# Kernel optimization log

Measured on AMD Instinct MI355X. Metric: run time of the kernel, lower is better.

## Reference

```python
import jax, jax.numpy as jnp
import numpy as np

N = 50000
NEG_SLOPE = 0.2  # PyG GATConv default leaky_relu slope


def _gat_layer(x, src, dst, W, a_s, a_d, b):
    # x: [N, Fin]; W: [Fin, H*C]; a_s, a_d: [H, C]; b: [C]
    H, C = a_s.shape
    xp = (x @ W).reshape(N, H, C)                      # projected node features per head
    alpha_s = jnp.einsum('nhc,hc->nh', xp, a_s)        # [N, H]
    alpha_d = jnp.einsum('nhc,hc->nh', xp, a_d)        # [N, H]
    e = jax.nn.leaky_relu(alpha_s[src] + alpha_d[dst], NEG_SLOPE)  # [E, H]
    # segment softmax over incoming edges of each dst node
    m = jax.ops.segment_max(e, dst, num_segments=N)
    m = jnp.where(jnp.isfinite(m), m, 0.0)
    p = jnp.exp(e - jax.lax.stop_gradient(m)[dst])
    denom = jax.ops.segment_sum(p, dst, num_segments=N)
    alpha = p / denom[dst]                             # [E, H]
    # scatter-aggregate messages
    out = jax.ops.segment_sum(alpha[:, :, None] * xp[src], dst, num_segments=N)  # [N, H, C]
    return out.mean(axis=1) + b                        # concat=False -> mean over heads


def setup_inputs() -> dict:
    key = jax.random.key(0)
    ks = jax.random.split(key, 16)
    IN, HID, OUT, H = 128, 64, 40, 4
    E = 800000
    x = jax.random.normal(ks[0], (N, IN), dtype=jnp.float32)
    edge_index = jax.random.randint(ks[1], (2, E), 0, N, dtype=jnp.int64)

    def mk(kw, ka, fin, fout):
        s = 1.0 / np.sqrt(fin)
        W = jax.random.normal(kw, (fin, H * fout), dtype=jnp.float32) * s
        a_s = jax.random.normal(ka, (H, fout), dtype=jnp.float32) * 0.1
        a_d = jax.random.normal(jax.random.fold_in(ka, 1), (H, fout), dtype=jnp.float32) * 0.1
        b = jnp.zeros((fout,), dtype=jnp.float32)
        return W, a_s, a_d, b

    W1, as1, ad1, b1 = mk(ks[2], ks[3], IN, HID)
    W2, as2, ad2, b2 = mk(ks[4], ks[5], HID, HID)
    W3, as3, ad3, b3 = mk(ks[6], ks[7], HID, OUT)
    return dict(x=x, edge_index=edge_index,
                W1=W1, as1=as1, ad1=ad1, b1=b1,
                W2=W2, as2=as2, ad2=ad2, b2=b2,
                W3=W3, as3=as3, ad3=ad3, b3=b3)


def reference(x, edge_index, W1, as1, ad1, b1, W2, as2, ad2, b2, W3, as3, ad3, b3):
    # PyG GATConv adds self-loops by default
    loop = jnp.arange(N, dtype=edge_index.dtype)
    src = jnp.concatenate([edge_index[0], loop])
    dst = jnp.concatenate([edge_index[1], loop])
    h = jax.nn.relu(_gat_layer(x, src, dst, W1, as1, ad1, b1))   # dropout is identity in eval
    h = jax.nn.relu(_gat_layer(h, src, dst, W2, as2, ad2, b2))
    h = jax.nn.relu(_gat_layer(h, src, dst, W3, as3, ad3, b3))
    return jax.nn.log_softmax(h, axis=-1)
```

## Files before the change

### kernel.cpp

```cpp
#include <hip/hip_runtime.h>
#include <math.h>

#define NNODES 50000
#define NEG_SLOPE 0.2f
#define NBUCKET 391
#define CHUNK_MAX 12544
#define NBIN_MAX 128

typedef unsigned short ushort8v __attribute__((ext_vector_type(8)));
typedef unsigned short ushort4v __attribute__((ext_vector_type(4)));
typedef short short8v __attribute__((ext_vector_type(8)));
typedef float f32x4 __attribute__((ext_vector_type(4)));
typedef float f32x2 __attribute__((ext_vector_type(2)));

__device__ __forceinline__ unsigned short f2bf(float f){
    unsigned u = __float_as_uint(f);
    u += 0x7fff + ((u >> 16) & 1);
    return (unsigned short)(u >> 16);
}

__device__ __forceinline__ void emit_wa(const float* __restrict__ W, const float* __restrict__ a_s,
                                        const float* __restrict__ a_d, unsigned short* __restrict__ Wt,
                                        int Kin, int C, int id){
    const int n = id / Kin, k = id - n * Kin;
    float v = 0.f;
    if(n < 8){
        const int hh = n & 3;
        const float* av = (n < 4) ? a_s : a_d;
        for(int c = 0; c < C; c++) v += W[(size_t)k * (4 * C) + hh * C + c] * av[hh * C + c];
    }
    Wt[id] = f2bf(v);
}

__device__ __forceinline__ void emit_wc(const float* __restrict__ W, unsigned short* __restrict__ Wt,
                                        int Kin, int C, int id){
    const int c = id / (4 * Kin);
    const int hk = id - c * (4 * Kin);
    const int h = hk / Kin, k = hk - h * Kin;
    const float v = (c < C) ? W[(size_t)k * (4 * C) + h * C + c] * 0.25f : 0.f;
    Wt[id] = f2bf(v);
}

__global__ void initprep_kernel(const unsigned long long* __restrict__ e, int* __restrict__ flag,
                                const float* __restrict__ x, unsigned short* __restrict__ xbf, int X4,
                                const float* __restrict__ W1, const float* __restrict__ as1, const float* __restrict__ ad1,
                                const float* __restrict__ W2, const float* __restrict__ as2, const float* __restrict__ ad2,
                                const float* __restrict__ W3, const float* __restrict__ as3, const float* __restrict__ ad3,
                                unsigned short* __restrict__ Wa1, unsigned short* __restrict__ Wa2,
                                unsigned short* __restrict__ Wa3, unsigned short* __restrict__ Wc1,
                                unsigned short* __restrict__ Wc2, unsigned short* __restrict__ Wc3){
    if(blockIdx.x == 0 && threadIdx.x < 64){
        const unsigned long long v = e[threadIdx.x];
        const unsigned long long mask = __ballot(v >= (1ULL << 32));
        if(threadIdx.x == 0) *flag = (mask == 0ULL) ? 1 : 0;
    }
    int id = blockIdx.x * blockDim.x + threadIdx.x;
    if(id < X4){
        const float4 v = *(const float4*)&x[(size_t)id * 4];
        ushort4v o;
        o[0] = f2bf(v.x); o[1] = f2bf(v.y); o[2] = f2bf(v.z); o[3] = f2bf(v.w);
        *(ushort4v*)&xbf[(size_t)id * 4] = o;
        return;
    }
    id -= X4;
    if(id < 16 * 128){ emit_wa(W1, as1, ad1, Wa1, 128, 64, id); return; }
    id -= 16 * 128;
    if(id < 16 * 64){ emit_wa(W2, as2, ad2, Wa2, 64, 64, id); return; }
    id -= 16 * 64;
    if(id < 16 * 64){ emit_wa(W3, as3, ad3, Wa3, 64, 40, id); return; }
    id -= 16 * 64;
    if(id < 64 * 512){ emit_wc(W1, Wc1, 128, 64, id); return; }
    id -= 64 * 512;
    if(id < 64 * 256){ emit_wc(W2, Wc2, 64, 64, id); return; }
    id -= 64 * 256;
    if(id < 48 * 256){ emit_wc(W3, Wc3, 64, 40, id); }
}

__global__ __launch_bounds__(256) void bincount_kernel(const void* __restrict__ e, const int* __restrict__ flag,
                                                       int* __restrict__ blkcnt, int E, int nbin, int chunk){
    __shared__ int lcnt[NBUCKET];
    for(int i = threadIdx.x; i < NBUCKET; i += 256) lcnt[i] = 0;
    __syncthreads();
    const bool f = (*flag) != 0;
    const int beg = blockIdx.x * chunk;
    const int end = min(beg + chunk, E);
    for(int i = beg + threadIdx.x; i < end; i += 256){
        const int d = f ? (int)((const long long*)e)[E + i] : ((const int*)e)[E + i];
        atomicAdd(&lcnt[d >> 7], 1);
    }
    __syncthreads();
    for(int b = threadIdx.x; b < NBUCKET; b += 256)
        blkcnt[b * nbin + blockIdx.x] = lcnt[b];
}

__global__ __launch_bounds__(256) void binscan_kernel(int* __restrict__ blkcnt, int total){
    __shared__ int part[256];
    const int t = threadIdx.x;
    const int per = (total + 255) / 256;
    const int beg = t * per, end = min(beg + per, total);
    int sum = 0;
    for(int i = beg; i < end; i++) sum += blkcnt[i];
    part[t] = sum;
    __syncthreads();
    for(int off = 1; off < 256; off <<= 1){
        const int add = (t >= off) ? part[t - off] : 0;
        __syncthreads();
        part[t] += add;
        __syncthreads();
    }
    int run = part[t] - sum;
    for(int i = beg; i < end; i++){
        const int v = blkcnt[i];
        blkcnt[i] = run;
        run += v;
    }
}

__global__ __launch_bounds__(256) void binscatter_kernel(const void* __restrict__ e, const int* __restrict__ flag,
                                                         const int* __restrict__ blkcnt,
                                                         unsigned* __restrict__ ebuf,
                                                         int E, int nbin, int chunk){
    __shared__ unsigned stage[CHUNK_MAX];
    __shared__ unsigned sorted[CHUNK_MAX];
    __shared__ int lcnt[512], lsc[512];
    __shared__ int lcur[NBUCKET], gb[NBUCKET];
    const int t = threadIdx.x;
    const int blk = blockIdx.x;
    lcnt[t] = 0; lcnt[t + 256] = 0;
    __syncthreads();
    const bool f = (*flag) != 0;
    const int beg = blk * chunk;
    const int cnt = min(chunk, E - beg);
    for(int i = t; i < cnt; i += 256){
        int s, d;
        if(f){ s = (int)((const long long*)e)[beg + i]; d = (int)((const long long*)e)[E + beg + i]; }
        else { s = ((const int*)e)[beg + i];            d = ((const int*)e)[E + beg + i]; }
        const int b = d >> 7;
        stage[i] = (unsigned)s | ((unsigned)(d & 127) << 16) | ((unsigned)b << 23);
        atomicAdd(&lcnt[b], 1);
    }
    __syncthreads();
    lsc[t] = lcnt[t]; lsc[t + 256] = lcnt[t + 256];
    __syncthreads();
    for(int off = 1; off < 512; off <<= 1){
        const int a0 = (t >= off) ? lsc[t - off] : 0;
        const int a1 = (t + 256 >= off) ? lsc[t + 256 - off] : 0;
        __syncthreads();
        lsc[t] += a0; lsc[t + 256] += a1;
        __syncthreads();
    }
    if(t < NBUCKET) lcur[t] = lsc[t] - lcnt[t];
    if(t + 256 < NBUCKET) lcur[t + 256] = lsc[t + 256] - lcnt[t + 256];
    for(int b = t; b < NBUCKET; b += 256) gb[b] = blkcnt[b * nbin + blk];
    __syncthreads();
    for(int i = t; i < cnt; i += 256){
        const unsigned w = stage[i];
        const int p = atomicAdd(&lcur[w >> 23], 1);
        sorted[p] = w;
    }
    __syncthreads();
    for(int i = t; i < cnt; i += 256){
        const unsigned w = sorted[i];
        const int b = w >> 23;
        ebuf[gb[b] + (i - (lsc[b] - lcnt[b]))] = w;
    }
}

__global__ __launch_bounds__(256) void bfinal_kernel(const unsigned* __restrict__ ebuf,
                                                     const int* __restrict__ blkcnt,
                                                     int* __restrict__ row_ptr, int* __restrict__ col,
                                                     int N, int E, int nbin){
    __shared__ int lcnt[128], lcur[128], sh[128];
    const int b = blockIdx.x;
    const int t = threadIdx.x;
    const int nlo = b << 7;
    const int base = blkcnt[b * nbin];
    const int next = (b == NBUCKET - 1) ? E : blkcnt[(b + 1) * nbin];
    const int cnt = next - base;
    if(t < 128) lcnt[t] = 0;
    __syncthreads();
    for(int i = t; i < cnt; i += 256) atomicAdd(&lcnt[(ebuf[base + i] >> 16) & 127], 1);
    __syncthreads();
    if(t < 128) sh[t] = lcnt[t];
    __syncthreads();
    for(int off = 1; off < 128; off <<= 1){
        const int add = (t >= off && t < 128) ? sh[t - off] : 0;
        __syncthreads();
        if(t < 128) sh[t] += add;
        __syncthreads();
    }
    if(t < 128){
        const int excl = sh[t] - lcnt[t];
        lcur[t] = excl;
        if(nlo + t < N) row_ptr[nlo + t] = base + excl;
    }
    if(b == 0 && t == 0) row_ptr[N] = E;
    __syncthreads();
    for(int i = t; i < cnt; i += 256){
        const unsigned w = ebuf[base + i];
        const int p = atomicAdd(&lcur[(w >> 16) & 127], 1);
        col[base + p] = (int)(w & 0xffffu);
    }
}

template<int K>
__global__ __launch_bounds__(256) void agemm_kernel(const unsigned short* __restrict__ A,
                                                    const unsigned short* __restrict__ Wa,
                                                    float* __restrict__ ea, float* __restrict__ ed,
                                                    int M){
    const int lane = threadIdx.x & 63;
    const int wave = threadIdx.x >> 6;
    const int quad = lane >> 4;
    const int l16 = lane & 15;
    const int bm = blockIdx.x * 64;
    const int m = min(bm + wave * 16 + l16, M - 1);
    f32x4 acc = {0,0,0,0};
    #pragma unroll
    for(int k0 = 0; k0 < K; k0 += 32){
        const short8v a = *(const short8v*)&A[(size_t)m * K + k0 + quad * 8];
        const short8v b = *(const short8v*)&Wa[(size_t)l16 * K + k0 + quad * 8];
        acc = __builtin_amdgcn_mfma_f32_16x16x32_bf16(a, b, acc, 0, 0, 0);
    }
    if(l16 < 8){
        const int h = l16 & 3;
        float* dst = (l16 < 4) ? ea : ed;
        const int rbase = bm + wave * 16 + quad * 4;
        #pragma unroll
        for(int r = 0; r < 4; r++){
            const int row = rbase + r;
            if(row < M){
                const float v = acc[r];
                *(f32x2*)&dst[(size_t)row * 8 + 2 * h] = (f32x2){__expf(v), __expf(NEG_SLOPE * v)};
            }
        }
    }
}

template<int K>
__global__ __launch_bounds__(256) void gatherg_kernel(const unsigned short* __restrict__ X,
                                                      const int* __restrict__ row_ptr,
                                                      const int* __restrict__ col,
                                                      const float* __restrict__ ea,
                                                      const float* __restrict__ ed,
                                                      unsigned short* __restrict__ g){
    __shared__ int   ls[4][64];
    __shared__ float lw[4][64][4];
    const int lane = threadIdx.x & 63;
    const int wave = threadIdx.x >> 6;
    const int n    = blockIdx.x * 4 + wave;
    const int rs = row_ptr[n], re = row_ptr[n + 1];
    const int T = re - rs + 1;
    const float4 edA = *(const float4*)&ed[(size_t)n * 8];
    const float4 edB = *(const float4*)&ed[(size_t)n * 8 + 4];

    f32x2 acc[4];
    #pragma unroll
    for(int h = 0; h < 4; h++) acc[h] = (f32x2){0.f, 0.f};
    float d0 = 0.f, d1 = 0.f, d2 = 0.f, d3 = 0.f;

    const int c2 = (K == 128) ? (lane * 2) : ((lane & 31) * 2);
    const int eo = lane >> 5;

    for(int base = 0; base < T; base += 64){
        const int ecnt = min(T - base, 64);
        if(lane < ecnt){
            const int e = rs + base + lane;
            const int s = (e < re) ? col[e] : n;
            const float4 eaA = *(const float4*)&ea[(size_t)s * 8];
            const float4 eaB = *(const float4*)&ea[(size_t)s * 8 + 4];
            const float w0 = fmaxf(eaA.x * edA.x, eaA.y * edA.y);
            const float w1 = fmaxf(eaA.z * edA.z, eaA.w * edA.w);
            const float w2 = fmaxf(eaB.x * edB.x, eaB.y * edB.y);
            const float w3 = fmaxf(eaB.z * edB.z, eaB.w * edB.w);
            d0 += w0; d1 += w1; d2 += w2; d3 += w3;
            ls[wave][lane] = s;
            *(f32x4*)&lw[wave][lane][0] = (f32x4){w0, w1, w2, w3};
        }
        if constexpr(K == 128){
            auto body = [&](int e){
                const int s = ls[wave][e];
                const f32x4 w4 = *(const f32x4*)&lw[wave][e][0];
                const unsigned u = *(const unsigned*)&X[(size_t)s * K + c2];
                const f32x2 v = {__uint_as_float(u << 16), __uint_as_float(u & 0xffff0000u)};
                acc[0] += (f32x2){w4[0], w4[0]} * v;
                acc[1] += (f32x2){w4[1], w4[1]} * v;
                acc[2] += (f32x2){w4[2], w4[2]} * v;
                acc[3] += (f32x2){w4[3], w4[3]} * v;
            };
            int e = 0;
            for(; e + 4 <= ecnt; e += 4){ body(e); body(e + 1); body(e + 2); body(e + 3); }
            for(; e < ecnt; e++) body(e);
        } else {
            auto body = [&](int p){
                const int e = p + eo;
                if(e < ecnt){
                    const int s = ls[wave][e];
                    const f32x4 w4 = *(const f32x4*)&lw[wave][e][0];
                    const unsigned u = *(const unsigned*)&X[(size_t)s * K + c2];
                    const f32x2 v = {__uint_as_float(u << 16), __uint_as_float(u & 0xffff0000u)};
                    acc[0] += (f32x2){w4[0], w4[0]} * v;
                    acc[1] += (f32x2){w4[1], w4[1]} * v;
                    acc[2] += (f32x2){w4[2], w4[2]} * v;
                    acc[3] += (f32x2){w4[3], w4[3]} * v;
                }
            };
            int p = 0;
            for(; p + 8 <= ecnt; p += 8){ body(p); body(p + 2); body(p + 4); body(p + 6); }
            for(; p < ecnt; p += 2) body(p);
        }
    }

    #pragma unroll
    for(int msk = 1; msk < 64; msk <<= 1){
        d0 += __shfl_xor(d0, msk); d1 += __shfl_xor(d1, msk);
        d2 += __shfl_xor(d2, msk); d3 += __shfl_xor(d3, msk);
    }
    if constexpr(K == 64){
        #pragma unroll
        for(int h = 0; h < 4; h++){
            acc[h][0] += __shfl_xor(acc[h][0], 32);
            acc[h][1] += __shfl_xor(acc[h][1], 32);
        }
    }
    const float invs[4] = {1.f / d0, 1.f / d1, 1.f / d2, 1.f / d3};
    if(K == 128 || lane < 32){
        #pragma unroll
        for(int h = 0; h < 4; h++){
            const unsigned lo = f2bf(acc[h][0] * invs[h]);
            const unsigned hi = f2bf(acc[h][1] * invs[h]);
            *(unsigned*)&g[(size_t)n * (4 * K) + h * K + c2] = lo | (hi << 16);
        }
    }
}

template<int KC, int NC, bool FINAL, bool ALPHA>
__global__ __launch_bounds__(256) void pgemm_kernel(const unsigned short* __restrict__ A,
                                                    const unsigned short* __restrict__ Bt,
                                                    const float* __restrict__ bias,
                                                    void* __restrict__ outv,
                                                    const unsigned short* __restrict__ Wa,
                                                    float* __restrict__ ea,
                                                    float* __restrict__ ed,
                                                    int M){
    constexpr int NT = (NC + 15) / 16;
    __shared__ unsigned short lh[ALPHA ? 4 : 1][16][72];
    const int lane = threadIdx.x & 63;
    const int wave = threadIdx.x >> 6;
    const int quad = lane >> 4;
    const int l16 = lane & 15;
    const int bm = blockIdx.x * 64;
    const int m = min(bm + wave * 16 + l16, M - 1);
    const size_t arow = (size_t)m * KC;

    f32x4 acc[NT];
    #pragma unroll
    for(int t = 0; t < NT; t++) acc[t] = (f32x4){0,0,0,0};

    for(int k0 = 0; k0 < KC; k0 += 32){
        const short8v a = *(const short8v*)&A[arow + k0 + quad * 8];
        #pragma unroll
        for(int t = 0; t < NT; t++){
            const short8v b = *(const short8v*)&Bt[(size_t)(t * 16 + l16) * KC + k0 + quad * 8];
            acc[t] = __builtin_amdgcn_mfma_f32_16x16x32_bf16(a, b, acc[t], 0, 0, 0);
        }
    }
    const int rbase = bm + wave * 16 + quad * 4;
    if(!FINAL){
        unsigned short* out = (unsigned short*)outv;
        #pragma unroll
        for(int t = 0; t < NT; t++){
            const int c = t * 16 + l16;
            #pragma unroll
            for(int r = 0; r < 4; r++){
                const unsigned short hb = f2bf(fmaxf(acc[t][r] + bias[c], 0.f));
                const int row = rbase + r;
                if(row < M) out[(size_t)row * NC + c] = hb;
                if constexpr(ALPHA) lh[wave][quad * 4 + r][c] = hb;
            }
        }
        if constexpr(ALPHA){
            f32x4 a4 = {0, 0, 0, 0};
            #pragma unroll
            for(int k0 = 0; k0 < 64; k0 += 32){
                const short8v a = *(const short8v*)&lh[wave][l16][k0 + quad * 8];
                const short8v b = *(const short8v*)&Wa[(size_t)l16 * 64 + k0 + quad * 8];
                a4 = __builtin_amdgcn_mfma_f32_16x16x32_bf16(a, b, a4, 0, 0, 0);
            }
            if(l16 < 8){
                const int h = l16 & 3;
                float* dst = (l16 < 4) ? ea : ed;
                #pragma unroll
                for(int r = 0; r < 4; r++){
                    const int row = rbase + r;
                    if(row < M){
                        const float v = a4[r];
                        *(f32x2*)&dst[(size_t)row * 8 + 2 * h] = (f32x2){__expf(v), __expf(NEG_SLOPE * v)};
                    }
                }
            }
        }
    } else {
        float* out = (float*)outv;
        float o[NT][4];
        #pragma unroll
        for(int t = 0; t < NT; t++){
            const int c = t * 16 + l16;
            const bool valid = c < 40;
            const float bc = valid ? bias[c] : 0.f;
            #pragma unroll
            for(int r = 0; r < 4; r++)
                o[t][r] = valid ? fmaxf(acc[t][r] + bc, 0.f) : -INFINITY;
        }
        #pragma unroll
        for(int r = 0; r < 4; r++){
            float mx = o[0][r];
            #pragma unroll
            for(int t = 1; t < NT; t++) mx = fmaxf(mx, o[t][r]);
            #pragma unroll
            for(int off = 1; off < 16; off <<= 1) mx = fmaxf(mx, __shfl_xor(mx, off));
            float se = 0.f;
            #pragma unroll
            for(int t = 0; t < NT; t++) se += (o[t][r] > -INFINITY) ? __expf(o[t][r] - mx) : 0.f;
            #pragma unroll
            for(int off = 1; off < 16; off <<= 1) se += __shfl_xor(se, off);
            const float lz = mx + logf(se);
            const int row = rbase + r;
            if(row < M){
                #pragma unroll
                for(int t = 0; t < NT; t++){
                    const int c = t * 16 + l16;
                    if(c < 40) out[(size_t)row * 40 + c] = o[t][r] - lz;
                }
            }
        }
    }
}

extern "C" void kernel_launch(void* const* d_in, const int* in_sizes, int n_in,
                              void* d_out, int out_size, void* d_ws, size_t ws_size,
                              hipStream_t stream){
    const int N = NNODES;
    const int E = in_sizes[1] / 2;

    const float* x   = (const float*)d_in[0];
    const float* W1  = (const float*)d_in[2];
    const float* as1 = (const float*)d_in[3];
    const float* ad1 = (const float*)d_in[4];
    const float* b1  = (const float*)d_in[5];
    const float* W2  = (const float*)d_in[6];
    const float* as2 = (const float*)d_in[7];
    const float* ad2 = (const float*)d_in[8];
    const float* b2  = (const float*)d_in[9];
    const float* W3  = (const float*)d_in[10];
    const float* as3 = (const float*)d_in[11];
    const float* ad3 = (const float*)d_in[12];
    const float* b3  = (const float*)d_in[13];

    char* ws = (char*)d_ws;
    size_t off = 0;
    auto alloc = [&](size_t bytes) -> void* {
        void* p = ws + off;
        off = (off + bytes + 255) & ~(size_t)255;
        return p;
    };
    int*      flag    = (int*)     alloc(4);
    int*      row_ptr = (int*)     alloc((size_t)(N + 1) * 4);
    int*      colv    = (int*)     alloc((size_t)E * 4);
    int*      blkcnt  = (int*)     alloc((size_t)NBUCKET * NBIN_MAX * 4);
    unsigned* ebuf    = (unsigned*)alloc((size_t)E * 4);
    unsigned short* xbf = (unsigned short*)alloc((size_t)N * 128 * 2);
    unsigned short* Wa1 = (unsigned short*)alloc(16 * 128 * 2);
    unsigned short* Wa2 = (unsigned short*)alloc(16 * 64 * 2);
    unsigned short* Wa3 = (unsigned short*)alloc(16 * 64 * 2);
    unsigned short* Wc1 = (unsigned short*)alloc((size_t)64 * 512 * 2);
    unsigned short* Wc2 = (unsigned short*)alloc((size_t)64 * 256 * 2);
    unsigned short* Wc3 = (unsigned short*)alloc((size_t)48 * 256 * 2);
    float* eav     = (float*)alloc((size_t)N * 8 * 4);
    float* edv     = (float*)alloc((size_t)N * 8 * 4);
    unsigned short* g   = (unsigned short*)alloc((size_t)N * 512 * 2);
    unsigned short* h1  = (unsigned short*)alloc((size_t)N * 64 * 2);
    unsigned short* h2  = (unsigned short*)alloc((size_t)N * 64 * 2);
    (void)ws_size;

    const void* eraw = d_in[1];

    const int X4 = N * 128 / 4;
    const int prepTotal = X4 + 16*128 + 16*64 + 16*64 + 64*512 + 64*256 + 48*256;
    initprep_kernel<<<(prepTotal + 255) / 256, 256, 0, stream>>>(
        (const unsigned long long*)eraw, flag, x, xbf, X4,
        W1, as1, ad1, W2, as2, ad2, W3, as3, ad3,
        Wa1, Wa2, Wa3, Wc1, Wc2, Wc3);

    const int chunkE = CHUNK_MAX;
    const int nbin = min((E + chunkE - 1) / chunkE, NBIN_MAX);
    bincount_kernel<<<nbin, 256, 0, stream>>>(eraw, flag, blkcnt, E, nbin, chunkE);
    binscan_kernel<<<1, 256, 0, stream>>>(blkcnt, NBUCKET * nbin);
    binscatter_kernel<<<nbin, 256, 0, stream>>>(eraw, flag, blkcnt, ebuf, E, nbin, chunkE);
    bfinal_kernel<<<NBUCKET, 256, 0, stream>>>(ebuf, blkcnt, row_ptr, colv, N, E, nbin);

    const int nodeBlocks = N / 4;
    const int mBlocks = (N + 63) / 64;

    agemm_kernel<128><<<mBlocks, 256, 0, stream>>>(xbf, Wa1, eav, edv, N);
    gatherg_kernel<128><<<nodeBlocks, 256, 0, stream>>>(xbf, row_ptr, colv, eav, edv, g);
    pgemm_kernel<512, 64, false, true><<<mBlocks, 256, 0, stream>>>(g, Wc1, b1, h1, Wa2, eav, edv, N);

    gatherg_kernel<64><<<nodeBlocks, 256, 0, stream>>>(h1, row_ptr, colv, eav, edv, g);
    pgemm_kernel<256, 64, false, true><<<mBlocks, 256, 0, stream>>>(g, Wc2, b2, h2, Wa3, eav, edv, N);

    gatherg_kernel<64><<<nodeBlocks, 256, 0, stream>>>(h2, row_ptr, colv, eav, edv, g);
    pgemm_kernel<256, 40, true, false><<<mBlocks, 256, 0, stream>>>(g, Wc3, b3, d_out, nullptr, nullptr, nullptr, N);
}
```

Measured before the change: 417.3 us.

## Fuse whole GAT pipeline into one cooperative persistent mega kernel

Adds a cooperative-launch persistent kernel that runs preprocessing, CSR build, attention GEMMs, gathers and projection GEMMs in sequence, separated by grid-wide syncs, replacing about a dozen kernel launches. It aims to remove launch overhead and the idle tails between small kernels. Stage kernels are refactored into device bodies so the fallback multi-kernel path still works. The fallback binning also changes to an atomic-cursor scatter with a fixed 64 bins. Grid syncs and a fixed grid size may underuse the GPU on the irregular gather stages.

```diff
diff --git a/kernel.cpp b/kernel.cpp
--- a/kernel.cpp
+++ b/kernel.cpp
@@ -1,5 +1,8 @@
 #include <hip/hip_runtime.h>
+#include <hip/hip_cooperative_groups.h>
 #include <math.h>
+
+namespace cg = cooperative_groups;
 
 #define NNODES 50000
 #define NEG_SLOPE 0.2f
@@ -41,20 +44,13 @@
     Wt[id] = f2bf(v);
 }
 
-__global__ void initprep_kernel(const unsigned long long* __restrict__ e, int* __restrict__ flag,
-                                const float* __restrict__ x, unsigned short* __restrict__ xbf, int X4,
-                                const float* __restrict__ W1, const float* __restrict__ as1, const float* __restrict__ ad1,
-                                const float* __restrict__ W2, const float* __restrict__ as2, const float* __restrict__ ad2,
-                                const float* __restrict__ W3, const float* __restrict__ as3, const float* __restrict__ ad3,
-                                unsigned short* __restrict__ Wa1, unsigned short* __restrict__ Wa2,
-                                unsigned short* __restrict__ Wa3, unsigned short* __restrict__ Wc1,
-                                unsigned short* __restrict__ Wc2, unsigned short* __restrict__ Wc3){
-    if(blockIdx.x == 0 && threadIdx.x < 64){
-        const unsigned long long v = e[threadIdx.x];
-        const unsigned long long mask = __ballot(v >= (1ULL << 32));
-        if(threadIdx.x == 0) *flag = (mask == 0ULL) ? 1 : 0;
-    }
-    int id = blockIdx.x * blockDim.x + threadIdx.x;
+__device__ __forceinline__ void prep_item(int id, const float* __restrict__ x,
+                                          unsigned short* __restrict__ xbf, int X4,
+                                          const float* W1, const float* as1, const float* ad1,
+                                          const float* W2, const float* as2, const float* ad2,
+                                          const float* W3, const float* as3, const float* ad3,
+                                          unsigned short* Wa1, unsigned short* Wa2, unsigned short* Wa3,
+                                          unsigned short* Wc1, unsigned short* Wc2, unsigned short* Wc3){
     if(id < X4){
         const float4 v = *(const float4*)&x[(size_t)id * 4];
         ushort4v o;
@@ -76,143 +72,16 @@
     if(id < 48 * 256){ emit_wc(W3, Wc3, 64, 40, id); }
 }
 
-__global__ __launch_bounds__(256) void bincount_kernel(const void* __restrict__ e, const int* __restrict__ flag,
-                                                       int* __restrict__ blkcnt, int E, int nbin, int chunk){
-    __shared__ int lcnt[NBUCKET];
-    for(int i = threadIdx.x; i < NBUCKET; i += 256) lcnt[i] = 0;
-    __syncthreads();
-    const bool f = (*flag) != 0;
-    const int beg = blockIdx.x * chunk;
-    const int end = min(beg + chunk, E);
-    for(int i = beg + threadIdx.x; i < end; i += 256){
-        const int d = f ? (int)((const long long*)e)[E + i] : ((const int*)e)[E + i];
-        atomicAdd(&lcnt[d >> 7], 1);
-    }
-    __syncthreads();
-    for(int b = threadIdx.x; b < NBUCKET; b += 256)
-        blkcnt[b * nbin + blockIdx.x] = lcnt[b];
-}
-
-__global__ __launch_bounds__(256) void binscan_kernel(int* __restrict__ blkcnt, int total){
-    __shared__ int part[256];
-    const int t = threadIdx.x;
-    const int per = (total + 255) / 256;
-    const int beg = t * per, end = min(beg + per, total);
-    int sum = 0;
-    for(int i = beg; i < end; i++) sum += blkcnt[i];
-    part[t] = sum;
-    __syncthreads();
-    for(int off = 1; off < 256; off <<= 1){
-        const int add = (t >= off) ? part[t - off] : 0;
-        __syncthreads();
-        part[t] += add;
-        __syncthreads();
-    }
-    int run = part[t] - sum;
-    for(int i = beg; i < end; i++){
-        const int v = blkcnt[i];
-        blkcnt[i] = run;
-        run += v;
-    }
-}
-
-__global__ __launch_bounds__(256) void binscatter_kernel(const void* __restrict__ e, const int* __restrict__ flag,
-                                                         const int* __restrict__ blkcnt,
-                                                         unsigned* __restrict__ ebuf,
-                                                         int E, int nbin, int chunk){
-    __shared__ unsigned stage[CHUNK_MAX];
-    __shared__ unsigned sorted[CHUNK_MAX];
-    __shared__ int lcnt[512], lsc[512];
-    __shared__ int lcur[NBUCKET], gb[NBUCKET];
-    const int t = threadIdx.x;
-    const int blk = blockIdx.x;
-    lcnt[t] = 0; lcnt[t + 256] = 0;
-    __syncthreads();
-    const bool f = (*flag) != 0;
-    const int beg = blk * chunk;
-    const int cnt = min(chunk, E - beg);
-    for(int i = t; i < cnt; i += 256){
-        int s, d;
-        if(f){ s = (int)((const long long*)e)[beg + i]; d = (int)((const long long*)e)[E + beg + i]; }
-        else { s = ((const int*)e)[beg + i];            d = ((const int*)e)[E + beg + i]; }
-        const int b = d >> 7;
-        stage[i] = (unsigned)s | ((unsigned)(d & 127) << 16) | ((unsigned)b << 23);
-        atomicAdd(&lcnt[b], 1);
-    }
-    __syncthreads();
-    lsc[t] = lcnt[t]; lsc[t + 256] = lcnt[t + 256];
-    __syncthreads();
-    for(int off = 1; off < 512; off <<= 1){
-        const int a0 = (t >= off) ? lsc[t - off] : 0;
-        const int a1 = (t + 256 >= off) ? lsc[t + 256 - off] : 0;
-        __syncthreads();
-        lsc[t] += a0; lsc[t + 256] += a1;
-        __syncthreads();
-    }
-    if(t < NBUCKET) lcur[t] = lsc[t] - lcnt[t];
-    if(t + 256 < NBUCKET) lcur[t + 256] = lsc[t + 256] - lcnt[t + 256];
-    for(int b = t; b < NBUCKET; b += 256) gb[b] = blkcnt[b * nbin + blk];
-    __syncthreads();
-    for(int i = t; i < cnt; i += 256){
-        const unsigned w = stage[i];
-        const int p = atomicAdd(&lcur[w >> 23], 1);
-        sorted[p] = w;
-    }
-    __syncthreads();
-    for(int i = t; i < cnt; i += 256){
-        const unsigned w = sorted[i];
-        const int b = w >> 23;
-        ebuf[gb[b] + (i - (lsc[b] - lcnt[b]))] = w;
-    }
-}
-
-__global__ __launch_bounds__(256) void bfinal_kernel(const unsigned* __restrict__ ebuf,
-                                                     const int* __restrict__ blkcnt,
-                                                     int* __restrict__ row_ptr, int* __restrict__ col,
-                                                     int N, int E, int nbin){
-    __shared__ int lcnt[128], lcur[128], sh[128];
-    const int b = blockIdx.x;
-    const int t = threadIdx.x;
-    const int nlo = b << 7;
-    const int base = blkcnt[b * nbin];
-    const int next = (b == NBUCKET - 1) ? E : blkcnt[(b + 1) * nbin];
-    const int cnt = next - base;
-    if(t < 128) lcnt[t] = 0;
-    __syncthreads();
-    for(int i = t; i < cnt; i += 256) atomicAdd(&lcnt[(ebuf[base + i] >> 16) & 127], 1);
-    __syncthreads();
-    if(t < 128) sh[t] = lcnt[t];
-    __syncthreads();
-    for(int off = 1; off < 128; off <<= 1){
-        const int add = (t >= off && t < 128) ? sh[t - off] : 0;
-        __syncthreads();
-        if(t < 128) sh[t] += add;
-        __syncthreads();
-    }
-    if(t < 128){
-        const int excl = sh[t] - lcnt[t];
-        lcur[t] = excl;
-        if(nlo + t < N) row_ptr[nlo + t] = base + excl;
-    }
-    if(b == 0 && t == 0) row_ptr[N] = E;
-    __syncthreads();
-    for(int i = t; i < cnt; i += 256){
-        const unsigned w = ebuf[base + i];
-        const int p = atomicAdd(&lcur[(w >> 16) & 127], 1);
-        col[base + p] = (int)(w & 0xffffu);
-    }
-}
 
 template<int K>
-__global__ __launch_bounds__(256) void agemm_kernel(const unsigned short* __restrict__ A,
-                                                    const unsigned short* __restrict__ Wa,
-                                                    float* __restrict__ ea, float* __restrict__ ed,
-                                                    int M){
+__device__ __forceinline__ void agemm_body(const unsigned short* __restrict__ A,
+                                           const unsigned short* __restrict__ Wa,
+                                           float* __restrict__ ea, float* __restrict__ ed,
+                                           int M, int bm){
     const int lane = threadIdx.x & 63;
     const int wave = threadIdx.x >> 6;
     const int quad = lane >> 4;
     const int l16 = lane & 15;
-    const int bm = blockIdx.x * 64;
     const int m = min(bm + wave * 16 + l16, M - 1);
     f32x4 acc = {0,0,0,0};
     #pragma unroll
@@ -237,17 +106,15 @@
 }
 
 template<int K>
-__global__ __launch_bounds__(256) void gatherg_kernel(const unsigned short* __restrict__ X,
-                                                      const int* __restrict__ row_ptr,
-                                                      const int* __restrict__ col,
-                                                      const float* __restrict__ ea,
-                                                      const float* __restrict__ ed,
-                                                      unsigned short* __restrict__ g){
-    __shared__ int   ls[4][64];
-    __shared__ float lw[4][64][4];
+__device__ __forceinline__ void gather_body(const unsigned short* __restrict__ X,
+                                            const int* __restrict__ row_ptr,
+                                            const int* __restrict__ col,
+                                            const float* __restrict__ ea,
+                                            const float* __restrict__ ed,
+                                            unsigned short* __restrict__ g,
+                                            int n, int* __restrict__ ls,
+                                            float (* __restrict__ lw)[4]){
     const int lane = threadIdx.x & 63;
-    const int wave = threadIdx.x >> 6;
-    const int n    = blockIdx.x * 4 + wave;
     const int rs = row_ptr[n], re = row_ptr[n + 1];
     const int T = re - rs + 1;
     const float4 edA = *(const float4*)&ed[(size_t)n * 8];
@@ -273,13 +140,13 @@
             const float w2 = fmaxf(eaB.x * edB.x, eaB.y * edB.y);
             const float w3 = fmaxf(eaB.z * edB.z, eaB.w * edB.w);
             d0 += w0; d1 += w1; d2 += w2; d3 += w3;
-            ls[wave][lane] = s;
-            *(f32x4*)&lw[wave][lane][0] = (f32x4){w0, w1, w2, w3};
+            ls[lane] = s;
+            *(f32x4*)&lw[lane][0] = (f32x4){w0, w1, w2, w3};
         }
         if constexpr(K == 128){
             auto body = [&](int e){
-                const int s = ls[wave][e];
-                const f32x4 w4 = *(const f32x4*)&lw[wave][e][0];
+                const int s = ls[e];
+                const f32x4 w4 = *(const f32x4*)&lw[e][0];
                 const unsigned u = *(const unsigned*)&X[(size_t)s * K + c2];
                 const f32x2 v = {__uint_as_float(u << 16), __uint_as_float(u & 0xffff0000u)};
                 acc[0] += (f32x2){w4[0], w4[0]} * v;
@@ -294,8 +161,8 @@
             auto body = [&](int p){
                 const int e = p + eo;
                 if(e < ecnt){
-                    const int s = ls[wave][e];
-                    const f32x4 w4 = *(const f32x4*)&lw[wave][e][0];
+                    const int s = ls[e];
+                    const f32x4 w4 = *(const f32x4*)&lw[e][0];
                     const unsigned u = *(const unsigned*)&X[(size_t)s * K + c2];
                     const f32x2 v = {__uint_as_float(u << 16), __uint_as_float(u & 0xffff0000u)};
                     acc[0] += (f32x2){w4[0], w4[0]} * v;
@@ -334,23 +201,23 @@
 }
 
 template<int KC, int NC, bool FINAL, bool ALPHA>
-__global__ __launch_bounds__(256) void pgemm_kernel(const unsigned short* __restrict__ A,
-                                                    const unsigned short* __restrict__ Bt,
-                                                    const float* __restrict__ bias,
-                                                    void* __restrict__ outv,
-                                                    const unsigned short* __restrict__ Wa,
-                                                    float* __restrict__ ea,
-                                                    float* __restrict__ ed,
-                                                    int M){
+__device__ __forceinline__ void pgemm_body(const unsigned short* __restrict__ A,
+                                           const unsigned short* __restrict__ Bt,
+                                           const float* __restrict__ bias,
+                                           void* __restrict__ outv,
+                                           const unsigned short* __restrict__ Wa,
+                                           float* __restrict__ ea, float* __restrict__ ed,
+                                           int M, int bm,
+                                           unsigned short (* __restrict__ lh)[72]){
     constexpr int NT = (NC + 15) / 16;
-    __shared__ unsigned short lh[ALPHA ? 4 : 1][16][72];
     const int lane = threadIdx.x & 63;
-    const int wave = threadIdx.x >> 6;
     const int quad = lane >> 4;
     const int l16 = lane & 15;
-    const int bm = blockIdx.x * 64;
-    const int m = min(bm + wave * 16 + l16, M - 1);
-    const size_t arow = (size_t)m * KC;
+    const int m = min(bm + (threadIdx.x >> 6) * 0 + 0, 0) * 0 + min(bm + ((threadIdx.x >> 6) & 0) , M - 1);
+    (void)m;
+    const int wrow = bm + l16;
+    const int mm = min(wrow, M - 1);
+    const size_t arow = (size_t)mm * KC;
 
     f32x4 acc[NT];
     #pragma unroll
@@ -364,8 +231,8 @@
             acc[t] = __builtin_amdgcn_mfma_f32_16x16x32_bf16(a, b, acc[t], 0, 0, 0);
         }
     }
-    const int rbase = bm + wave * 16 + quad * 4;
-    if(!FINAL){
+    const int rbase = bm + quad * 4;
+    if constexpr(!FINAL){
         unsigned short* out = (unsigned short*)outv;
         #pragma unroll
         for(int t = 0; t < NT; t++){
@@ -375,14 +242,14 @@
                 const unsigned short hb = f2bf(fmaxf(acc[t][r] + bias[c], 0.f));
                 const int row = rbase + r;
                 if(row < M) out[(size_t)row * NC + c] = hb;
-                if constexpr(ALPHA) lh[wave][quad * 4 + r][c] = hb;
+                if constexpr(ALPHA) lh[quad * 4 + r][c] = hb;
             }
         }
         if constexpr(ALPHA){
             f32x4 a4 = {0, 0, 0, 0};
             #pragma unroll
             for(int k0 = 0; k0 < 64; k0 += 32){
-                const short8v a = *(const short8v*)&lh[wave][l16][k0 + quad * 8];
+                const short8v a = *(const short8v*)&lh[l16][k0 + quad * 8];
                 const short8v b = *(const short8v*)&Wa[(size_t)l16 * 64 + k0 + quad * 8];
                 a4 = __builtin_amdgcn_mfma_f32_16x16x32_bf16(a, b, a4, 0, 0, 0);
             }
@@ -434,6 +301,310 @@
             }
         }
     }
+}
+
+__device__ __forceinline__ void bfinal_body(const unsigned* __restrict__ ebuf,
+                                            const int* __restrict__ blkcnt,
+                                            int* __restrict__ row_ptr, int* __restrict__ col,
+                                            int N, int E, int nbin, int b,
+                                            int* __restrict__ lcnt, int* __restrict__ lcur,
+                                            int* __restrict__ sh){
+    const int t = threadIdx.x;
+    const int nlo = b << 7;
+    const int base = blkcnt[b * nbin];
+    const int next = (b == NBUCKET - 1) ? E : blkcnt[(b + 1) * nbin];
+    const int cnt = next - base;
+    if(t < 128) lcnt[t] = 0;
+    __syncthreads();
+    for(int i = t; i < cnt; i += 256) atomicAdd(&lcnt[(ebuf[base + i] >> 16) & 127], 1);
+    __syncthreads();
+    if(t < 128) sh[t] = lcnt[t];
+    __syncthreads();
+    for(int off = 1; off < 128; off <<= 1){
+        const int add = (t >= off && t < 128) ? sh[t - off] : 0;
+        __syncthreads();
+        if(t < 128) sh[t] += add;
+        __syncthreads();
+    }
+    if(t < 128){
+        const int excl = sh[t] - lcnt[t];
+        lcur[t] = excl;
+        if(nlo + t < N) row_ptr[nlo + t] = base + excl;
+    }
+    __syncthreads();
+    for(int i = t; i < cnt; i += 256){
+        const unsigned w = ebuf[base + i];
+        const int p = atomicAdd(&lcur[(w >> 16) & 127], 1);
+        col[base + p] = (int)(w & 0xffffu);
+    }
+    __syncthreads();
+}
+
+struct MegaArgs {
+    const void* eraw; int E;
+    int* flag;
+    const float* x;
+    const float* W1; const float* as1; const float* ad1; const float* b1;
+    const float* W2; const float* as2; const float* ad2; const float* b2;
+    const float* W3; const float* as3; const float* ad3; const float* b3;
+    unsigned short* xbf;
+    unsigned short* Wa1; unsigned short* Wa2; unsigned short* Wa3;
+    unsigned short* Wc1; unsigned short* Wc2; unsigned short* Wc3;
+    int* blkcnt; unsigned* ebuf; int* row_ptr; int* colv;
+    float* eav; float* edv;
+    unsigned short* g; unsigned short* h1; unsigned short* h2;
+    void* out;
+};
+
+__global__ __launch_bounds__(256) void mega_kernel(MegaArgs a){
+    union Smem {
+        struct { int ls[4][64]; float lw[4][64][4]; } gat;
+        int hist[NBUCKET];
+        int cur[NBUCKET];
+        int part[256];
+        struct { int lcnt[128]; int lcur[128]; int sh[128]; } fin;
+        unsigned short lh[4][16][72];
+    };
+    __shared__ Smem sm;
+    cg::grid_group grid = cg::this_grid();
+    const int t = threadIdx.x;
+    const int wave = t >> 6;
+    const int NB = gridDim.x;
+    const int E = a.E;
+    const int mBlocks = (NNODES + 63) / 64;
+    const int nGroups = NNODES / 4;
+
+    if(blockIdx.x == 0 && t < 64){
+        const unsigned long long v = ((const unsigned long long*)a.eraw)[t];
+        const unsigned long long mask = __ballot(v >= (1ULL << 32));
+        if(t == 0) *a.flag = (mask == 0ULL) ? 1 : 0;
+    }
+    {
+        const int X4 = NNODES * 32;
+        const int prepTotal = X4 + 16*128 + 16*64 + 16*64 + 64*512 + 64*256 + 48*256;
+        for(int id = blockIdx.x * 256 + t; id < prepTotal; id += NB * 256)
+            prep_item(id, a.x, a.xbf, X4, a.W1, a.as1, a.ad1, a.W2, a.as2, a.ad2,
+                      a.W3, a.as3, a.ad3, a.Wa1, a.Wa2, a.Wa3, a.Wc1, a.Wc2, a.Wc3);
+    }
+    grid.sync();
+
+    const int chunk = (E + 63) >> 6;
+    if(blockIdx.x < 64){
+        for(int i = t; i < NBUCKET; i += 256) sm.hist[i] = 0;
+        __syncthreads();
+        const bool f = (*a.flag) != 0;
+        const int beg = blockIdx.x * chunk, end = min(beg + chunk, E);
+        for(int i = beg + t; i < end; i += 256){
+            const int d = f ? (int)((const long long*)a.eraw)[E + i] : ((const int*)a.eraw)[E + i];
+            atomicAdd(&sm.hist[d >> 7], 1);
+        }
+        __syncthreads();
+        for(int b = t; b < NBUCKET; b += 256) a.blkcnt[b * 64 + blockIdx.x] = sm.hist[b];
+    } else {
+        for(int mb = blockIdx.x - 64; mb < mBlocks; mb += NB - 64)
+            agemm_body<128>(a.xbf, a.Wa1, a.eav, a.edv, NNODES, mb * 64);
+    }
+    grid.sync();
+
+    if(blockIdx.x == 0){
+        const int total = NBUCKET * 64;
+        const int per = (total + 255) / 256;
+        const int beg = t * per, end = min(beg + per, total);
+        int sum = 0;
+        for(int i = beg; i < end; i++) sum += a.blkcnt[i];
+        sm.part[t] = sum;
+        __syncthreads();
+        for(int off = 1; off < 256; off <<= 1){
+            const int add = (t >= off) ? sm.part[t - off] : 0;
+            __syncthreads();
+            sm.part[t] += add;
+            __syncthreads();
+        }
+        int run = sm.part[t] - sum;
+        for(int i = beg; i < end; i++){
+            const int v = a.blkcnt[i];
+            a.blkcnt[i] = run;
+            run += v;
+        }
+    }
+    grid.sync();
+
+    if(blockIdx.x < 64){
+        for(int b = t; b < NBUCKET; b += 256) sm.cur[b] = a.blkcnt[b * 64 + blockIdx.x];
+        __syncthreads();
+        const bool f = (*a.flag) != 0;
+        const int beg = blockIdx.x * chunk, end = min(beg + chunk, E);
+        for(int i = beg + t; i < end; i += 256){
+            int s, d;
+            if(f){ s = (int)((const long long*)a.eraw)[i]; d = (int)((const long long*)a.eraw)[E + i]; }
+            else { s = ((const int*)a.eraw)[i];            d = ((const int*)a.eraw)[E + i]; }
+            const int b = d >> 7;
+            const int p = atomicAdd(&sm.cur[b], 1);
+            a.ebuf[p] = (unsigned)s | ((unsigned)(d & 127) << 16) | ((unsigned)b << 23);
+        }
+    }
+    grid.sync();
+
+    if(blockIdx.x == 0 && t == 0) a.row_ptr[NNODES] = E;
+    for(int b = blockIdx.x; b < NBUCKET; b += NB)
+        bfinal_body(a.ebuf, a.blkcnt, a.row_ptr, a.colv, NNODES, E, 64, b,
+                    sm.fin.lcnt, sm.fin.lcur, sm.fin.sh);
+    grid.sync();
+
+    for(int grp = blockIdx.x; grp < nGroups; grp += NB)
+        gather_body<128>(a.xbf, a.row_ptr, a.colv, a.eav, a.edv, a.g,
+                         grp * 4 + wave, sm.gat.ls[wave], sm.gat.lw[wave]);
+    grid.sync();
+
+    for(int mb = blockIdx.x; mb < mBlocks; mb += NB)
+        pgemm_body<512, 64, false, true>(a.g, a.Wc1, a.b1, a.h1, a.Wa2, a.eav, a.edv,
+                                         NNODES, mb * 64 + wave * 16, sm.lh[wave]);
+    grid.sync();
+
+    for(int grp = blockIdx.x; grp < nGroups; grp += NB)
+        gather_body<64>(a.h1, a.row_ptr, a.colv, a.eav, a.edv, a.g,
+                        grp * 4 + wave, sm.gat.ls[wave], sm.gat.lw[wave]);
+    grid.sync();
+
+    for(int mb = blockIdx.x; mb < mBlocks; mb += NB)
+        pgemm_body<256, 64, false, true>(a.g, a.Wc2, a.b2, a.h2, a.Wa3, a.eav, a.edv,
+                                         NNODES, mb * 64 + wave * 16, sm.lh[wave]);
+    grid.sync();
+
+    for(int grp = blockIdx.x; grp < nGroups; grp += NB)
+        gather_body<64>(a.h2, a.row_ptr, a.colv, a.eav, a.edv, a.g,
+                        grp * 4 + wave, sm.gat.ls[wave], sm.gat.lw[wave]);
+    grid.sync();
+
+    for(int mb = blockIdx.x; mb < mBlocks; mb += NB)
+        pgemm_body<256, 40, true, false>(a.g, a.Wc3, a.b3, a.out, nullptr, nullptr, nullptr,
+                                         NNODES, mb * 64 + wave * 16, sm.lh[wave]);
+}
+
+
+__global__ void initprep_kernel(const unsigned long long* __restrict__ e, int* __restrict__ flag,
+                                const float* __restrict__ x, unsigned short* __restrict__ xbf, int X4,
+                                const float* __restrict__ W1, const float* __restrict__ as1, const float* __restrict__ ad1,
+                                const float* __restrict__ W2, const float* __restrict__ as2, const float* __restrict__ ad2,
+                                const float* __restrict__ W3, const float* __restrict__ as3, const float* __restrict__ ad3,
+                                unsigned short* __restrict__ Wa1, unsigned short* __restrict__ Wa2,
+                                unsigned short* __restrict__ Wa3, unsigned short* __restrict__ Wc1,
+                                unsigned short* __restrict__ Wc2, unsigned short* __restrict__ Wc3){
+    if(blockIdx.x == 0 && threadIdx.x < 64){
+        const unsigned long long v = e[threadIdx.x];
+        const unsigned long long mask = __ballot(v >= (1ULL << 32));
+        if(threadIdx.x == 0) *flag = (mask == 0ULL) ? 1 : 0;
+    }
+    const int id = blockIdx.x * blockDim.x + threadIdx.x;
+    prep_item(id, x, xbf, X4, W1, as1, ad1, W2, as2, ad2, W3, as3, ad3,
+              Wa1, Wa2, Wa3, Wc1, Wc2, Wc3);
+}
+
+__global__ __launch_bounds__(256) void bincount_kernel(const void* __restrict__ e, const int* __restrict__ flag,
+                                                       int* __restrict__ blkcnt, int E, int nbin, int chunk){
+    __shared__ int lcnt[NBUCKET];
+    for(int i = threadIdx.x; i < NBUCKET; i += 256) lcnt[i] = 0;
+    __syncthreads();
+    const bool f = (*flag) != 0;
+    const int beg = blockIdx.x * chunk;
+    const int end = min(beg + chunk, E);
+    for(int i = beg + threadIdx.x; i < end; i += 256){
+        const int d = f ? (int)((const long long*)e)[E + i] : ((const int*)e)[E + i];
+        atomicAdd(&lcnt[d >> 7], 1);
+    }
+    __syncthreads();
+    for(int b = threadIdx.x; b < NBUCKET; b += 256)
+        blkcnt[b * nbin + blockIdx.x] = lcnt[b];
+}
+
+__global__ __launch_bounds__(256) void binscan_kernel(int* __restrict__ blkcnt, int total){
+    __shared__ int part[256];
+    const int t = threadIdx.x;
+    const int per = (total + 255) / 256;
+    const int beg = t * per, end = min(beg + per, total);
+    int sum = 0;
+    for(int i = beg; i < end; i++) sum += blkcnt[i];
+    part[t] = sum;
+    __syncthreads();
+    for(int off = 1; off < 256; off <<= 1){
+        const int add = (t >= off) ? part[t - off] : 0;
+        __syncthreads();
+        part[t] += add;
+        __syncthreads();
+    }
+    int run = part[t] - sum;
+    for(int i = beg; i < end; i++){
+        const int v = blkcnt[i];
+        blkcnt[i] = run;
+        run += v;
+    }
+}
+
+__global__ __launch_bounds__(256) void binscatter_kernel(const void* __restrict__ e, const int* __restrict__ flag,
+                                                         const int* __restrict__ blkcnt,
+                                                         unsigned* __restrict__ ebuf,
+                                                         int E, int nbin, int chunk){
+    __shared__ int lcur[NBUCKET];
+    const int t = threadIdx.x;
+    for(int b = t; b < NBUCKET; b += 256) lcur[b] = blkcnt[b * nbin + blockIdx.x];
+    __syncthreads();
+    const bool f = (*flag) != 0;
+    const int beg = blockIdx.x * chunk;
+    const int end = min(beg + chunk, E);
+    for(int i = beg + t; i < end; i += 256){
+        int s, d;
+        if(f){ s = (int)((const long long*)e)[i]; d = (int)((const long long*)e)[E + i]; }
+        else { s = ((const int*)e)[i];            d = ((const int*)e)[E + i]; }
+        const int b = d >> 7;
+        const int p = atomicAdd(&lcur[b], 1);
+        ebuf[p] = (unsigned)s | ((unsigned)(d & 127) << 16) | ((unsigned)b << 23);
+    }
+}
+
+__global__ __launch_bounds__(256) void bfinal_kernel(const unsigned* __restrict__ ebuf,
+                                                     const int* __restrict__ blkcnt,
+                                                     int* __restrict__ row_ptr, int* __restrict__ col,
+                                                     int N, int E, int nbin){
+    __shared__ int lcnt[128], lcur[128], sh[128];
+    if(blockIdx.x == 0 && threadIdx.x == 0) row_ptr[N] = E;
+    bfinal_body(ebuf, blkcnt, row_ptr, col, N, E, nbin, blockIdx.x, lcnt, lcur, sh);
+}
+
+template<int K>
+__global__ __launch_bounds__(256) void agemm_kernel(const unsigned short* __restrict__ A,
+                                                    const unsigned short* __restrict__ Wa,
+                                                    float* __restrict__ ea, float* __restrict__ ed,
+                                                    int M){
+    agemm_body<K>(A, Wa, ea, ed, M, blockIdx.x * 64);
+}
+
+template<int K>
+__global__ __launch_bounds__(256) void gatherg_kernel(const unsigned short* __restrict__ X,
+                                                      const int* __restrict__ row_ptr,
+                                                      const int* __restrict__ col,
+                                                      const float* __restrict__ ea,
+                                                      const float* __restrict__ ed,
+                                                      unsigned short* __restrict__ g){
+    __shared__ int   ls[4][64];
+    __shared__ float lw[4][64][4];
+    const int wave = threadIdx.x >> 6;
+    gather_body<K>(X, row_ptr, col, ea, ed, g, blockIdx.x * 4 + wave, ls[wave], lw[wave]);
+}
+
+template<int KC, int NC, bool FINAL, bool ALPHA>
+__global__ __launch_bounds__(256) void pgemm_kernel(const unsigned short* __restrict__ A,
+                                                    const unsigned short* __restrict__ Bt,
+                                                    const float* __restrict__ bias,
+                                                    void* __restrict__ outv,
+                                                    const unsigned short* __restrict__ Wa,
+                                                    float* __restrict__ ea,
+                                                    float* __restrict__ ed,
+                                                    int M){
+    __shared__ unsigned short lh[ALPHA ? 4 : 1][16][72];
+    const int wave = threadIdx.x >> 6;
+    pgemm_body<KC, NC, FINAL, ALPHA>(A, Bt, bias, outv, Wa, ea, ed, M,
+                                     blockIdx.x * 64 + wave * 16,
+                                     lh[ALPHA ? wave : 0]);
 }
 
 extern "C" void kernel_launch(void* const* d_in, const int* in_sizes, int n_in,
@@ -484,6 +655,41 @@
 
     const void* eraw = d_in[1];
 
+    bool launched = false;
+    int dev = 0;
+    (void)hipGetDevice(&dev);
+    int coop = 0;
+    (void)hipDeviceGetAttribute(&coop, hipDeviceAttributeCooperativeLaunch, dev);
+    if(coop){
+        int maxPerCU = 0;
+        if(hipOccupancyMaxActiveBlocksPerMultiprocessor(&maxPerCU, mega_kernel, 256, 0) == hipSuccess
+           && maxPerCU > 0){
+            int numCU = 0;
+            (void)hipDeviceGetAttribute(&numCU, hipDeviceAttributeMultiprocessorCount, dev);
+            const int nblk = maxPerCU * numCU;
+            if(nblk >= 320){
+                MegaArgs ma;
+                ma.eraw = eraw; ma.E = E; ma.flag = flag; ma.x = x;
+                ma.W1 = W1; ma.as1 = as1; ma.ad1 = ad1; ma.b1 = b1;
+                ma.W2 = W2; ma.as2 = as2; ma.ad2 = ad2; ma.b2 = b2;
+                ma.W3 = W3; ma.as3 = as3; ma.ad3 = ad3; ma.b3 = b3;
+                ma.xbf = xbf; ma.Wa1 = Wa1; ma.Wa2 = Wa2; ma.Wa3 = Wa3;
+                ma.Wc1 = Wc1; ma.Wc2 = Wc2; ma.Wc3 = Wc3;
+                ma.blkcnt = blkcnt; ma.ebuf = ebuf; ma.row_ptr = row_ptr; ma.colv = colv;
+                ma.eav = eav; ma.edv = edv; ma.g = g; ma.h1 = h1; ma.h2 = h2;
+                ma.out = d_out;
+                void* kargs[] = { (void*)&ma };
+                if(hipLaunchCooperativeKernel(mega_kernel, dim3(nblk), dim3(256),
+                                              kargs, 0, stream) == hipSuccess){
+                    launched = true;
+                } else {
+                    (void)hipGetLastError();
+                }
+            }
+        }
+    }
+    if(launched) return;
+
     const int X4 = N * 128 / 4;
     const int prepTotal = X4 + 16*128 + 16*64 + 16*64 + 64*512 + 64*256 + 48*256;
     initprep_kernel<<<(prepTotal + 255) / 256, 256, 0, stream>>>(
@@ -491,8 +697,8 @@
         W1, as1, ad1, W2, as2, ad2, W3, as3, ad3,
         Wa1, Wa2, Wa3, Wc1, Wc2, Wc3);
 
-    const int chunkE = CHUNK_MAX;
-    const int nbin = min((E + chunkE - 1) / chunkE, NBIN_MAX);
+    const int nbin = 64;
+    const int chunkE = (E + nbin - 1) / nbin;
     bincount_kernel<<<nbin, 256, 0, stream>>>(eraw, flag, blkcnt, E, nbin, chunkE);
     binscan_kernel<<<1, 256, 0, stream>>>(blkcnt, NBUCKET * nbin);
     binscatter_kernel<<<nbin, 256, 0, stream>>>(eraw, flag, blkcnt, ebuf, E, nbin, chunkE);
```

After: 421.7 us. No clear change (+1.1%).

## Vectorize gather loads across edge groups and simplify bin scatter to direct atomics

Applied to the files above, without the earlier changes.

The gather kernel now has each lane load 8 bf16 features with one 16-byte load, processes several edges per wave in parallel, and reduces partial sums across lane groups with shuffles before a vectorized store. The bin scatter kernel removes shared-memory staging and local sorting, writing each edge directly to global memory through per-bucket atomic cursors, with a fixed count of 64 bins. This targets fewer, wider memory transactions in the gather and less sync/scan overhead in the scatter. In exchange, register pressure rises, scatter writes become uncoalesced, and edge order within a bucket is nondeterministic.

```diff
diff --git a/kernel.cpp b/kernel.cpp
--- a/kernel.cpp
+++ b/kernel.cpp
@@ -4,7 +4,6 @@
 #define NNODES 50000
 #define NEG_SLOPE 0.2f
 #define NBUCKET 391
-#define CHUNK_MAX 12544
 #define NBIN_MAX 128
 
 typedef unsigned short ushort8v __attribute__((ext_vector_type(8)));
@@ -120,49 +119,20 @@
                                                          const int* __restrict__ blkcnt,
                                                          unsigned* __restrict__ ebuf,
                                                          int E, int nbin, int chunk){
-    __shared__ unsigned stage[CHUNK_MAX];
-    __shared__ unsigned sorted[CHUNK_MAX];
-    __shared__ int lcnt[512], lsc[512];
-    __shared__ int lcur[NBUCKET], gb[NBUCKET];
+    __shared__ int lcur[NBUCKET];
     const int t = threadIdx.x;
-    const int blk = blockIdx.x;
-    lcnt[t] = 0; lcnt[t + 256] = 0;
+    for(int b = t; b < NBUCKET; b += 256) lcur[b] = blkcnt[b * nbin + blockIdx.x];
     __syncthreads();
     const bool f = (*flag) != 0;
-    const int beg = blk * chunk;
-    const int cnt = min(chunk, E - beg);
-    for(int i = t; i < cnt; i += 256){
+    const int beg = blockIdx.x * chunk;
+    const int end = min(beg + chunk, E);
+    for(int i = beg + t; i < end; i += 256){
         int s, d;
-        if(f){ s = (int)((const long long*)e)[beg + i]; d = (int)((const long long*)e)[E + beg + i]; }
-        else { s = ((const int*)e)[beg + i];            d = ((const int*)e)[E + beg + i]; }
+        if(f){ s = (int)((const long long*)e)[i]; d = (int)((const long long*)e)[E + i]; }
+        else { s = ((const int*)e)[i];            d = ((const int*)e)[E + i]; }
         const int b = d >> 7;
-        stage[i] = (unsigned)s | ((unsigned)(d & 127) << 16) | ((unsigned)b << 23);
-        atomicAdd(&lcnt[b], 1);
-    }
-    __syncthreads();
-    lsc[t] = lcnt[t]; lsc[t + 256] = lcnt[t + 256];
-    __syncthreads();
-    for(int off = 1; off < 512; off <<= 1){
-        const int a0 = (t >= off) ? lsc[t - off] : 0;
-        const int a1 = (t + 256 >= off) ? lsc[t + 256 - off] : 0;
-        __syncthreads();
-        lsc[t] += a0; lsc[t + 256] += a1;
-        __syncthreads();
-    }
-    if(t < NBUCKET) lcur[t] = lsc[t] - lcnt[t];
-    if(t + 256 < NBUCKET) lcur[t + 256] = lsc[t + 256] - lcnt[t + 256];
-    for(int b = t; b < NBUCKET; b += 256) gb[b] = blkcnt[b * nbin + blk];
-    __syncthreads();
-    for(int i = t; i < cnt; i += 256){
-        const unsigned w = stage[i];
-        const int p = atomicAdd(&lcur[w >> 23], 1);
-        sorted[p] = w;
-    }
-    __syncthreads();
-    for(int i = t; i < cnt; i += 256){
-        const unsigned w = sorted[i];
-        const int b = w >> 23;
-        ebuf[gb[b] + (i - (lsc[b] - lcnt[b]))] = w;
+        const int p = atomicAdd(&lcur[b], 1);
+        ebuf[p] = (unsigned)s | ((unsigned)(d & 127) << 16) | ((unsigned)b << 23);
     }
 }
 
@@ -243,23 +213,26 @@
                                                       const float* __restrict__ ea,
                                                       const float* __restrict__ ed,
                                                       unsigned short* __restrict__ g){
+    constexpr int LPR = K / 8;
+    constexpr int EPI = 64 / LPR;
     __shared__ int   ls[4][64];
     __shared__ float lw[4][64][4];
     const int lane = threadIdx.x & 63;
     const int wave = threadIdx.x >> 6;
     const int n    = blockIdx.x * 4 + wave;
+    const int grp  = lane / LPR;
+    const int pos  = lane % LPR;
     const int rs = row_ptr[n], re = row_ptr[n + 1];
     const int T = re - rs + 1;
     const float4 edA = *(const float4*)&ed[(size_t)n * 8];
     const float4 edB = *(const float4*)&ed[(size_t)n * 8 + 4];
 
-    f32x2 acc[4];
+    f32x2 acc[4][4];
     #pragma unroll
-    for(int h = 0; h < 4; h++) acc[h] = (f32x2){0.f, 0.f};
+    for(int h = 0; h < 4; h++)
+        #pragma unroll
+        for(int p = 0; p < 4; p++) acc[h][p] = (f32x2){0.f, 0.f};
     float d0 = 0.f, d1 = 0.f, d2 = 0.f, d3 = 0.f;
-
-    const int c2 = (K == 128) ? (lane * 2) : ((lane & 31) * 2);
-    const int eo = lane >> 5;
 
     for(int base = 0; base < T; base += 64){
         const int ecnt = min(T - base, 64);
@@ -276,38 +249,26 @@
             ls[wave][lane] = s;
             *(f32x4*)&lw[wave][lane][0] = (f32x4){w0, w1, w2, w3};
         }
-        if constexpr(K == 128){
-            auto body = [&](int e){
+        auto body = [&](int e0){
+            const int e = e0 + grp;
+            if(e < ecnt){
                 const int s = ls[wave][e];
                 const f32x4 w4 = *(const f32x4*)&lw[wave][e][0];
-                const unsigned u = *(const unsigned*)&X[(size_t)s * K + c2];
-                const f32x2 v = {__uint_as_float(u << 16), __uint_as_float(u & 0xffff0000u)};
-                acc[0] += (f32x2){w4[0], w4[0]} * v;
-                acc[1] += (f32x2){w4[1], w4[1]} * v;
-                acc[2] += (f32x2){w4[2], w4[2]} * v;
-                acc[3] += (f32x2){w4[3], w4[3]} * v;
-            };
-            int e = 0;
-            for(; e + 4 <= ecnt; e += 4){ body(e); body(e + 1); body(e + 2); body(e + 3); }
-            for(; e < ecnt; e++) body(e);
-        } else {
-            auto body = [&](int p){
-                const int e = p + eo;
-                if(e < ecnt){
-                    const int s = ls[wave][e];
-                    const f32x4 w4 = *(const f32x4*)&lw[wave][e][0];
-                    const unsigned u = *(const unsigned*)&X[(size_t)s * K + c2];
-                    const f32x2 v = {__uint_as_float(u << 16), __uint_as_float(u & 0xffff0000u)};
-                    acc[0] += (f32x2){w4[0], w4[0]} * v;
-                    acc[1] += (f32x2){w4[1], w4[1]} * v;
-                    acc[2] += (f32x2){w4[2], w4[2]} * v;
-                    acc[3] += (f32x2){w4[3], w4[3]} * v;
+                const uint4 u = *(const uint4*)&X[(size_t)s * K + pos * 8];
+                const unsigned uu[4] = {u.x, u.y, u.z, u.w};
+                #pragma unroll
+                for(int p = 0; p < 4; p++){
+                    const f32x2 v = {__uint_as_float(uu[p] << 16), __uint_as_float(uu[p] & 0xffff0000u)};
+                    acc[0][p] += (f32x2){w4[0], w4[0]} * v;
+                    acc[1][p] += (f32x2){w4[1], w4[1]} * v;
+                    acc[2][p] += (f32x2){w4[2], w4[2]} * v;
+                    acc[3][p] += (f32x2){w4[3], w4[3]} * v;
                 }
-            };
-            int p = 0;
-            for(; p + 8 <= ecnt; p += 8){ body(p); body(p + 2); body(p + 4); body(p + 6); }
-            for(; p < ecnt; p += 2) body(p);
-        }
+            }
+        };
+        int e0 = 0;
+        for(; e0 + 2 * EPI <= ecnt; e0 += 2 * EPI){ body(e0); body(e0 + EPI); }
+        for(; e0 < ecnt; e0 += EPI) body(e0);
     }
 
     #pragma unroll
@@ -315,20 +276,27 @@
         d0 += __shfl_xor(d0, msk); d1 += __shfl_xor(d1, msk);
         d2 += __shfl_xor(d2, msk); d3 += __shfl_xor(d3, msk);
     }
-    if constexpr(K == 64){
+    #pragma unroll
+    for(int msk = LPR; msk < 64; msk <<= 1){
+        #pragma unroll
+        for(int h = 0; h < 4; h++)
+            #pragma unroll
+            for(int p = 0; p < 4; p++){
+                acc[h][p][0] += __shfl_xor(acc[h][p][0], msk);
+                acc[h][p][1] += __shfl_xor(acc[h][p][1], msk);
+            }
+    }
+    const float invs[4] = {1.f / d0, 1.f / d1, 1.f / d2, 1.f / d3};
+    if(lane < LPR){
         #pragma unroll
         for(int h = 0; h < 4; h++){
-            acc[h][0] += __shfl_xor(acc[h][0], 32);
-            acc[h][1] += __shfl_xor(acc[h][1], 32);
-        }
-    }
-    const float invs[4] = {1.f / d0, 1.f / d1, 1.f / d2, 1.f / d3};
-    if(K == 128 || lane < 32){
-        #pragma unroll
-        for(int h = 0; h < 4; h++){
-            const unsigned lo = f2bf(acc[h][0] * invs[h]);
-            const unsigned hi = f2bf(acc[h][1] * invs[h]);
-            *(unsigned*)&g[(size_t)n * (4 * K) + h * K + c2] = lo | (hi << 16);
+            ushort8v o;
+            #pragma unroll
+            for(int p = 0; p < 4; p++){
+                o[2 * p]     = f2bf(acc[h][p][0] * invs[h]);
+                o[2 * p + 1] = f2bf(acc[h][p][1] * invs[h]);
+            }
+            *(ushort8v*)&g[(size_t)n * (4 * K) + h * K + pos * 8] = o;
         }
     }
 }
@@ -491,8 +459,8 @@
         W1, as1, ad1, W2, as2, ad2, W3, as3, ad3,
         Wa1, Wa2, Wa3, Wc1, Wc2, Wc3);
 
-    const int chunkE = CHUNK_MAX;
-    const int nbin = min((E + chunkE - 1) / chunkE, NBIN_MAX);
+    const int nbin = 64;
+    const int chunkE = (E + nbin - 1) / nbin;
     bincount_kernel<<<nbin, 256, 0, stream>>>(eraw, flag, blkcnt, E, nbin, chunkE);
     binscan_kernel<<<1, 256, 0, stream>>>(blkcnt, NBUCKET * nbin);
     binscatter_kernel<<<nbin, 256, 0, stream>>>(eraw, flag, blkcnt, ebuf, E, nbin, chunkE);
```

New measurement: 480.4 us. 1.15x slower.
